# Performance work log

Measured on AMD Instinct MI355X. Metric: run time of the kernel, lower is better.

The kernel has to match this reference:

```python
import jax, jax.numpy as jnp
import numpy as np

S, B, D = 2048, 1, 4096
H, HKV, DH = 32, 8, 128
THETA = 10000.0


def _rope_tables(seq_len, dim, theta):
    inv_freq = 1.0 / (theta ** (jnp.arange(0, dim, 2, dtype=jnp.float32) / dim))
    freqs = jnp.arange(seq_len, dtype=jnp.float32)[:, None] * inv_freq[None, :]  # [S, DH/2]
    return jnp.cos(freqs), jnp.sin(freqs)


def _apply_rope(x, cos, sin):
    # x: [B, H, S, DH]; non-interleaved (flash_attn interleaved=False) rotation
    half = x.shape[-1] // 2
    x1, x2 = x[..., :half], x[..., half:]
    c = cos[None, None, :, :]
    s = sin[None, None, :, :]
    return jnp.concatenate([x1 * c - x2 * s, x2 * c + x1 * s], axis=-1)


def setup_inputs() -> dict:
    key = jax.random.key(0)
    k1, k2, k3 = jax.random.split(key, 3)
    hidden_states = jax.random.normal(k1, (S, B, D), dtype=jnp.float32)
    W_qkv = jax.random.normal(k2, (D, (H + 2 * HKV) * DH), dtype=jnp.float32) * 0.02
    W_o = jax.random.normal(k3, (H * DH, D), dtype=jnp.float32) * 0.02
    sequence_mask = jnp.ones((B, S), dtype=jnp.int32)
    return {"hidden_states": hidden_states, "sequence_mask": sequence_mask,
            "W_qkv": W_qkv, "W_o": W_o}


def reference(hidden_states, sequence_mask, W_qkv, W_o):
    s, b, _ = hidden_states.shape
    qkv = hidden_states @ W_qkv  # [S, B, (H+2*HKV)*DH]
    q, k, v = jnp.split(qkv, [H * DH, H * DH + HKV * DH], axis=-1)
    q = q.reshape(s, b, H, DH).transpose(1, 2, 0, 3)    # [B, H, S, DH]
    k = k.reshape(s, b, HKV, DH).transpose(1, 2, 0, 3)  # [B, HKV, S, DH]
    v = v.reshape(s, b, HKV, DH).transpose(1, 2, 0, 3)

    cos, sin = _rope_tables(s, DH, THETA)
    q = _apply_rope(q, cos, sin)
    k = _apply_rope(k, cos, sin)

    # GQA: repeat kv heads
    rep = H // HKV
    k = jnp.repeat(k, rep, axis=1)  # [B, H, S, DH]
    v = jnp.repeat(v, rep, axis=1)

    scale = 1.0 / jnp.sqrt(jnp.asarray(DH, dtype=q.dtype))
    scores = jnp.einsum('bhqd,bhkd->bhqk', q, k) * scale
    causal = jnp.tril(jnp.ones((s, s), dtype=bool))
    scores = jnp.where(causal[None, None, :, :], scores, jnp.finfo(scores.dtype).min)
    attn = jax.nn.softmax(scores, axis=-1)
    ctx = jnp.einsum('bhqk,bhkd->bhqd', attn, v)  # [B, H, S, DH]
    ctx = ctx.transpose(2, 0, 1, 3).reshape(s, b, H * DH)  # [S, B, H*DH]
    out = ctx @ W_o  # [S, B, D]
    return out
```

## Files before the change

kernel.cpp:

```cpp
#include <hip/hip_runtime.h>

typedef unsigned short u16;
typedef __bf16 bf16x8 __attribute__((ext_vector_type(8)));
typedef float f32x4 __attribute__((ext_vector_type(4)));
typedef u16 u16x4 __attribute__((ext_vector_type(4)));

constexpr int SEQ = 2048;
constexpr int NQKV = 6144;

__device__ __forceinline__ float bf2f(u16 x) {
    unsigned int u = ((unsigned int)x) << 16;
    return __builtin_bit_cast(float, u);
}
__device__ __forceinline__ u16 f2bf(float f) {
    unsigned int u = __builtin_bit_cast(unsigned int, f);
    u += 0x7FFF + ((u >> 16) & 1);
    return (u16)(u >> 16);
}

__device__ __forceinline__ void gload16(const void* g, void* l) {
    void* gg = const_cast<void*>(g);
    __builtin_amdgcn_global_load_lds(
        (__attribute__((address_space(1))) void*)gg,
        (__attribute__((address_space(3))) void*)l, 16, 0, 0);
}

__device__ __forceinline__ void gatebar(int G) {
    if (G == 8) asm volatile("s_waitcnt vmcnt(8)" ::: "memory");
    else if (G == 4) asm volatile("s_waitcnt vmcnt(4)" ::: "memory");
    else asm volatile("s_waitcnt vmcnt(0)" ::: "memory");
    __builtin_amdgcn_sched_barrier(0);
    __builtin_amdgcn_s_barrier();
    __builtin_amdgcn_sched_barrier(0);
}

__global__ void rope_table_k(float* __restrict__ tab) {
    int idx = blockIdx.x * 256 + threadIdx.x;
    if (idx >= SEQ * 64) return;
    int s = idx >> 6;
    int i = idx & 63;
    float invf = expf(-(float)i * (float)(1.0 / 64.0) * logf(10000.0f));
    float ang = (float)s * invf;
    float sv, cv;
    sincosf(ang, &sv, &cv);
    tab[idx * 2] = cv;
    tab[idx * 2 + 1] = sv;
}

__global__ __launch_bounds__(256) void cast_k(const float* __restrict__ src,
                                              u16* __restrict__ dst, int n4) {
    int i = blockIdx.x * 256 + threadIdx.x;
    if (i >= n4) return;
    f32x4 v = *(const f32x4*)&src[(size_t)i * 4];
    u16x4 o;
#pragma unroll
    for (int j = 0; j < 4; ++j) o[j] = f2bf(v[j]);
    *(u16x4*)&dst[(size_t)i * 4] = o;
}

__global__ __launch_bounds__(256) void transpose_cast_k(const float* __restrict__ src,
                                                        u16* __restrict__ dst, int R, int C) {
    __shared__ u16 tile[64][65];
    int t = threadIdx.x;
    int bx = blockIdx.x, by = blockIdx.y;
    int r0 = by * 64, c0 = bx * 64;
#pragma unroll
    for (int it = 0; it < 4; ++it) {
        int row = it * 16 + (t >> 4);
        int col = (t & 15) * 4;
        f32x4 v = *(const f32x4*)&src[(size_t)(r0 + row) * C + c0 + col];
        tile[row][col] = f2bf(v[0]); tile[row][col + 1] = f2bf(v[1]);
        tile[row][col + 2] = f2bf(v[2]); tile[row][col + 3] = f2bf(v[3]);
    }
    __syncthreads();
#pragma unroll
    for (int it = 0; it < 4; ++it) {
        int orow = it * 16 + (t >> 4);
        int ocol = (t & 15) * 4;
        u16x4 v;
        v[0] = tile[ocol][orow]; v[1] = tile[ocol + 1][orow];
        v[2] = tile[ocol + 2][orow]; v[3] = tile[ocol + 3][orow];
        *(u16x4*)&dst[(size_t)(c0 + orow) * R + r0 + ocol] = v;
    }
}

__global__ __launch_bounds__(256) void transpose_vt_k(const u16* __restrict__ QKV,
                                                      u16* __restrict__ VTg) {
    __shared__ u16 tile[64][65];
    int t = threadIdx.x;
    int s0 = blockIdx.x * 64;
    int hv = blockIdx.y >> 1;
    int d0 = (blockIdx.y & 1) * 64;
    const u16* src = QKV + (size_t)s0 * NQKV + 5120 + hv * 128 + d0;
#pragma unroll
    for (int it = 0; it < 4; ++it) {
        int row = it * 16 + (t >> 4);
        int col = (t & 15) * 4;
        u16x4 v = *(const u16x4*)&src[(size_t)row * NQKV + col];
        tile[row][col] = v[0]; tile[row][col + 1] = v[1];
        tile[row][col + 2] = v[2]; tile[row][col + 3] = v[3];
    }
    __syncthreads();
    u16* dst = VTg + (size_t)hv * 128 * SEQ + (size_t)d0 * SEQ + s0;
#pragma unroll
    for (int it = 0; it < 4; ++it) {
        int orow = it * 16 + (t >> 4);
        int ocol = (t & 15) * 4;
        u16x4 v;
        v[0] = tile[ocol][orow]; v[1] = tile[ocol + 1][orow];
        v[2] = tile[ocol + 2][orow]; v[3] = tile[ocol + 3][orow];
        *(u16x4*)&dst[(size_t)orow * SEQ + ocol] = v;
    }
}

__global__ __launch_bounds__(512, 2) void gemm1_big_k(const u16* __restrict__ A,
                                                      const u16* __restrict__ BT,
                                                      u16* __restrict__ C) {
    constexpr int K = 4096, N = 6144;
    constexpr int SBUF = 57344;
    __shared__ alignas(16) char lds[2 * SBUF];

    int t = threadIdx.x;
    int lane = t & 63, w = t >> 6;
    int wr = w >> 2, wc = w & 3;
    int l15 = lane & 15, l4 = lane >> 4;

    int wg = blockIdx.x;
    int xcd = wg & 7, j = wg >> 3;
    int bm = ((xcd >> 2) << 2) + (j >> 3);
    int bn = ((xcd & 3) << 3) + (j & 7);

    const u16* Ab = A + (size_t)bm * 256 * K;
    const u16* Bb = BT + (size_t)bn * 192 * K;

    const u16* ga[4]; int da[4];
#pragma unroll
    for (int i = 0; i < 4; ++i) {
        int c = t + i * 512;
        int row = c >> 3;
        int ch = (c & 7) ^ (row & 7);
        ga[i] = Ab + (size_t)row * K + ch * 8;
        da[i] = c * 16;
    }
    const u16* gb[3]; int db[3];
#pragma unroll
    for (int i = 0; i < 3; ++i) {
        int c = t + i * 512;
        int row = c >> 3;
        int ch = (c & 7) ^ (row & 7);
        gb[i] = Bb + (size_t)row * K + ch * 8;
        db[i] = 32768 + c * 16;
    }

    auto stage = [&](int kt) {
        char* L = lds + (kt & 1) * SBUF;
        int ko = kt * 64;
#pragma unroll
        for (int i = 0; i < 4; ++i) gload16(ga[i] + ko, L + da[i]);
#pragma unroll
        for (int i = 0; i < 3; ++i) gload16(gb[i] + ko, L + db[i]);
    };

    f32x4 acc[8][3];
#pragma unroll
    for (int i = 0; i < 8; ++i)
#pragma unroll
        for (int j2 = 0; j2 < 3; ++j2) acc[i][j2] = f32x4{0.f, 0.f, 0.f, 0.f};

    int arow[8];
#pragma unroll
    for (int fm = 0; fm < 8; ++fm) arow[fm] = wr * 128 + fm * 16 + l15;
    int brow[3];
#pragma unroll
    for (int fn = 0; fn < 3; ++fn) brow[fn] = wc * 48 + fn * 16 + l15;

    stage(0);
    gatebar(0);

    for (int kt = 0; kt < 64; ++kt) {
        const u16* L = (const u16*)(lds + (kt & 1) * SBUF);
        if (kt + 1 < 64) stage(kt + 1);
        bf16x8 bf[3][2];
#pragma unroll
        for (int fn = 0; fn < 3; ++fn)
#pragma unroll
            for (int kk = 0; kk < 2; ++kk) {
                int ch = (kk * 4 + l4) ^ (brow[fn] & 7);
                bf[fn][kk] = *(const bf16x8*)&L[16384 + brow[fn] * 64 + ch * 8];
            }
#pragma unroll
        for (int p = 0; p < 4; ++p) {
            bf16x8 af[2][2];
#pragma unroll
            for (int f2 = 0; f2 < 2; ++f2)
#pragma unroll
                for (int kk = 0; kk < 2; ++kk) {
                    int r = arow[p * 2 + f2];
                    int ch = (kk * 4 + l4) ^ (r & 7);
                    af[f2][kk] = *(const bf16x8*)&L[r * 64 + ch * 8];
                }
            __builtin_amdgcn_s_setprio(1);
#pragma unroll
            for (int f2 = 0; f2 < 2; ++f2)
#pragma unroll
                for (int kk = 0; kk < 2; ++kk)
#pragma unroll
                    for (int fn = 0; fn < 3; ++fn)
                        acc[p * 2 + f2][fn] = __builtin_amdgcn_mfma_f32_16x16x32_bf16(
                            af[f2][kk], bf[fn][kk], acc[p * 2 + f2][fn], 0, 0, 0);
            __builtin_amdgcn_s_setprio(0);
        }
        gatebar(0);
    }

#pragma unroll
    for (int fm = 0; fm < 8; ++fm)
#pragma unroll
        for (int fn = 0; fn < 3; ++fn)
#pragma unroll
            for (int i = 0; i < 4; ++i) {
                int row = bm * 256 + wr * 128 + fm * 16 + l4 * 4 + i;
                int col = bn * 192 + wc * 48 + fn * 16 + l15;
                C[(size_t)row * N + col] = f2bf(acc[fm][fn][i]);
            }
}

__global__ __launch_bounds__(512, 2) void gemm2_big_k(const u16* __restrict__ A,
                                                      const u16* __restrict__ BT,
                                                      float* __restrict__ C) {
    constexpr int K = 4096, N = 4096;
    constexpr int SBUF = 49152;
    __shared__ alignas(16) char lds[2 * SBUF];

    int t = threadIdx.x;
    int lane = t & 63, w = t >> 6;
    int wr = w >> 2, wc = w & 3;
    int l15 = lane & 15, l4 = lane >> 4;

    int wg = blockIdx.x;
    int xcd = wg & 7, j = wg >> 3;
    int bm = ((xcd >> 2) << 2) + (j >> 3);
    int bn = ((xcd & 3) << 3) + (j & 7);

    const u16* Ab = A + (size_t)bm * 256 * K;
    const u16* Bb = BT + (size_t)bn * 128 * K;

    const u16* ga[4]; int da[4];
#pragma unroll
    for (int i = 0; i < 4; ++i) {
        int c = t + i * 512;
        int row = c >> 3;
        int ch = (c & 7) ^ (row & 7);
        ga[i] = Ab + (size_t)row * K + ch * 8;
        da[i] = c * 16;
    }
    const u16* gb[2]; int db[2];
#pragma unroll
    for (int i = 0; i < 2; ++i) {
        int c = t + i * 512;
        int row = c >> 3;
        int ch = (c & 7) ^ (row & 7);
        gb[i] = Bb + (size_t)row * K + ch * 8;
        db[i] = 32768 + c * 16;
    }

    auto stage = [&](int kt) {
        char* L = lds + (kt & 1) * SBUF;
        int ko = kt * 64;
#pragma unroll
        for (int i = 0; i < 4; ++i) gload16(ga[i] + ko, L + da[i]);
#pragma unroll
        for (int i = 0; i < 2; ++i) gload16(gb[i] + ko, L + db[i]);
    };

    f32x4 acc[8][2];
#pragma unroll
    for (int i = 0; i < 8; ++i)
#pragma unroll
        for (int j2 = 0; j2 < 2; ++j2) acc[i][j2] = f32x4{0.f, 0.f, 0.f, 0.f};

    int arow[8];
#pragma unroll
    for (int fm = 0; fm < 8; ++fm) arow[fm] = wr * 128 + fm * 16 + l15;
    int brow[2];
#pragma unroll
    for (int fn = 0; fn < 2; ++fn) brow[fn] = wc * 32 + fn * 16 + l15;

    stage(0);
    gatebar(0);

    for (int kt = 0; kt < 64; ++kt) {
        const u16* L = (const u16*)(lds + (kt & 1) * SBUF);
        if (kt + 1 < 64) stage(kt + 1);
        bf16x8 bf[2][2];
#pragma unroll
        for (int fn = 0; fn < 2; ++fn)
#pragma unroll
            for (int kk = 0; kk < 2; ++kk) {
                int ch = (kk * 4 + l4) ^ (brow[fn] & 7);
                bf[fn][kk] = *(const bf16x8*)&L[16384 + brow[fn] * 64 + ch * 8];
            }
#pragma unroll
        for (int p = 0; p < 4; ++p) {
            bf16x8 af[2][2];
#pragma unroll
            for (int f2 = 0; f2 < 2; ++f2)
#pragma unroll
                for (int kk = 0; kk < 2; ++kk) {
                    int r = arow[p * 2 + f2];
                    int ch = (kk * 4 + l4) ^ (r & 7);
                    af[f2][kk] = *(const bf16x8*)&L[r * 64 + ch * 8];
                }
            __builtin_amdgcn_s_setprio(1);
#pragma unroll
            for (int f2 = 0; f2 < 2; ++f2)
#pragma unroll
                for (int kk = 0; kk < 2; ++kk)
#pragma unroll
                    for (int fn = 0; fn < 2; ++fn)
                        acc[p * 2 + f2][fn] = __builtin_amdgcn_mfma_f32_16x16x32_bf16(
                            af[f2][kk], bf[fn][kk], acc[p * 2 + f2][fn], 0, 0, 0);
            __builtin_amdgcn_s_setprio(0);
        }
        gatebar(0);
    }

#pragma unroll
    for (int fm = 0; fm < 8; ++fm)
#pragma unroll
        for (int fn = 0; fn < 2; ++fn)
#pragma unroll
            for (int i = 0; i < 4; ++i) {
                int row = bm * 256 + wr * 128 + fm * 16 + l4 * 4 + i;
                int col = bn * 128 + wc * 32 + fn * 16 + l15;
                C[(size_t)row * N + col] = acc[fm][fn][i];
            }
}

__global__ __launch_bounds__(256) void repack_rope_k(const u16* __restrict__ QKV,
                                                     const float* __restrict__ tab,
                                                     u16* __restrict__ Qo, u16* __restrict__ Ko) {
    int idx = blockIdx.x * 256 + threadIdx.x;
    int i4 = (idx & 15) * 4;
    int su = idx >> 4;
    int u = su % 40;
    int s = su / 40;
    const float* tp = tab + (s * 64 + i4) * 2;
    f32x4 t0 = *(const f32x4*)tp;
    f32x4 t1 = *(const f32x4*)(tp + 4);
    float cv[4] = {t0[0], t0[2], t1[0], t1[2]};
    float sv[4] = {t0[1], t0[3], t1[1], t1[3]};
    const u16* base;
    u16* ob;
    if (u < 32) {
        base = QKV + (size_t)s * NQKV + u * 128;
        ob = Qo + ((size_t)u * SEQ + s) * 128;
    } else {
        base = QKV + (size_t)s * NQKV + 4096 + (u - 32) * 128;
        ob = Ko + ((size_t)(u - 32) * SEQ + s) * 128;
    }
    u16x4 x1 = *(const u16x4*)(base + i4);
    u16x4 x2 = *(const u16x4*)(base + 64 + i4);
    u16x4 o1, o2;
#pragma unroll
    for (int j = 0; j < 4; ++j) {
        float a = bf2f(x1[j]), b = bf2f(x2[j]);
        o1[j] = f2bf(a * cv[j] - b * sv[j]);
        o2[j] = f2bf(b * cv[j] + a * sv[j]);
    }
    *(u16x4*)(ob + i4) = o1;
    *(u16x4*)(ob + 64 + i4) = o2;
}

__global__ __launch_bounds__(512) void attn_k(const u16* __restrict__ Qg,
                                              const u16* __restrict__ Kg,
                                              const u16* __restrict__ VTg,
                                              u16* __restrict__ ctx) {
    constexpr float SCL2 = 0.08838834764831845f * 1.44269504088896340736f;
    constexpr float THR = 11.5f;
    __shared__ alignas(16) u16 Klds[2][128 * 128];
    __shared__ alignas(16) u16 VTl[2][128 * 128];
    __shared__ alignas(16) u16 Plds[8 * 16 * 72];

    int t = threadIdx.x;
    int lane = t & 63, w = t >> 6;
    int l15 = lane & 15, l4 = lane >> 4;
    int bx = blockIdx.x;
    int h = blockIdx.y, hkv = h >> 2;
    const u16* Kh = Kg + (size_t)hkv * SEQ * 128;
    const u16* Vh = VTg + (size_t)hkv * 128 * SEQ;
    u16* Pw = &Plds[w * 1152];

    int kr[4], kchs[4];
#pragma unroll
    for (int i2 = 0; i2 < 4; ++i2) {
        int c = t + i2 * 512;
        kr[i2] = c >> 4;
        kchs[i2] = (c & 15) ^ (kr[i2] & 7);
    }
    int vd[4], vchs[4];
#pragma unroll
    for (int i2 = 0; i2 < 4; ++i2) {
        int c = t + i2 * 512;
        vd[i2] = c >> 4;
        vchs[i2] = (c & 15) ^ (vd[i2] & 7);
    }

    int q0 = bx * 128;
    int ntA = bx + 1;

    bf16x8 qf[4];
    f32x4 o[8];
    float m_i[4], l_i[4];

    auto kvbase = [&](int tt) { return (tt < ntA ? tt : tt - ntA) << 7; };
    auto load_q = [&]() {
        const u16* Qh = Qg + ((size_t)h * SEQ + q0 + w * 16 + l15) * 128;
#pragma unroll
        for (int ks = 0; ks < 4; ++ks) qf[ks] = *(const bf16x8*)(Qh + ks * 32 + l4 * 8);
    };
    auto reset_acc = [&]() {
#pragma unroll
        for (int nf = 0; nf < 8; ++nf) o[nf] = f32x4{0.f, 0.f, 0.f, 0.f};
#pragma unroll
        for (int i = 0; i < 4; ++i) { m_i[i] = -3.0e38f; l_i[i] = 0.f; }
    };
    auto write_ctx = [&]() {
        float inv[4];
#pragma unroll
        for (int i = 0; i < 4; ++i) {
            float rs = l_i[i];
            rs += __shfl_xor(rs, 1);
            rs += __shfl_xor(rs, 2);
            rs += __shfl_xor(rs, 4);
            rs += __shfl_xor(rs, 8);
            inv[i] = 1.0f / rs;
        }
#pragma unroll
        for (int nf = 0; nf < 8; ++nf)
#pragma unroll
            for (int i = 0; i < 4; ++i) {
                int qrow = q0 + w * 16 + l4 * 4 + i;
                ctx[(size_t)qrow * 4096 + h * 128 + nf * 16 + l15] = f2bf(o[nf][i] * inv[i]);
            }
    };
    auto stage = [&](int tt) {
        int kv0 = kvbase(tt);
        const u16* Kt = Kh + (size_t)kv0 * 128;
        char* kb = (char*)Klds[tt & 1];
        char* vb = (char*)VTl[tt & 1];
#pragma unroll
        for (int i2 = 0; i2 < 4; ++i2)
            gload16(Kt + kr[i2] * 128 + kchs[i2] * 8, kb + (size_t)(t + i2 * 512) * 16);
#pragma unroll
        for (int i2 = 0; i2 < 4; ++i2)
            gload16(Vh + (size_t)vd[i2] * SEQ + kv0 + vchs[i2] * 8,
                    vb + (size_t)(t + i2 * 512) * 16);
    };

    load_q();
    reset_acc();
    stage(0);

    for (int tt = 0; tt < 17; ++tt) {
        __builtin_amdgcn_s_barrier();
        __builtin_amdgcn_sched_barrier(0);
        bool nxt = (tt + 1 < 17);
        if (nxt) stage(tt + 1);
        gatebar(nxt ? 8 : 0);
        if (tt == ntA) {
            write_ctx();
            q0 = (15 - bx) * 128;
            load_q();
            reset_acc();
        }

        int b = tt & 1;
        int kv0 = kvbase(tt);
        const u16* KL = Klds[b];
        const u16* VL = VTl[b];

        f32x4 sa[8];
#pragma unroll
        for (int cg = 0; cg < 8; ++cg) {
            sa[cg] = f32x4{0.f, 0.f, 0.f, 0.f};
            int row = cg * 16 + l15;
#pragma unroll
            for (int ks = 0; ks < 4; ++ks) {
                int chs = (ks * 4 + l4) ^ (row & 7);
                bf16x8 kf = *(const bf16x8*)&KL[row * 128 + chs * 8];
                sa[cg] = __builtin_amdgcn_mfma_f32_16x16x32_bf16(qf[ks], kf, sa[cg], 0, 0, 0);
            }
        }
#pragma unroll
        for (int cg = 0; cg < 8; ++cg)
#pragma unroll
            for (int i = 0; i < 4; ++i) sa[cg][i] *= SCL2;
        if (kv0 + 127 > q0 + w * 16) {
#pragma unroll
            for (int cg = 0; cg < 8; ++cg) {
                int col = kv0 + cg * 16 + l15;
#pragma unroll
                for (int i = 0; i < 4; ++i) {
                    int qrow = q0 + w * 16 + l4 * 4 + i;
                    if (col > qrow) sa[cg][i] = -3.0e38f;
                }
            }
        }
        float lmx[4];
#pragma unroll
        for (int i = 0; i < 4; ++i) {
            float a0 = fmaxf(fmaxf(sa[0][i], sa[1][i]), fmaxf(sa[2][i], sa[3][i]));
            float a1 = fmaxf(fmaxf(sa[4][i], sa[5][i]), fmaxf(sa[6][i], sa[7][i]));
            lmx[i] = fmaxf(a0, a1);
        }
        bool defer = __all((lmx[0] <= m_i[0] + THR) & (lmx[1] <= m_i[1] + THR) &
                           (lmx[2] <= m_i[2] + THR) & (lmx[3] <= m_i[3] + THR));
        if (!defer) {
            float corr[4];
#pragma unroll
            for (int i = 0; i < 4; ++i) {
                float m0 = lmx[i];
                m0 = fmaxf(m0, __shfl_xor(m0, 1));
                m0 = fmaxf(m0, __shfl_xor(m0, 2));
                m0 = fmaxf(m0, __shfl_xor(m0, 4));
                m0 = fmaxf(m0, __shfl_xor(m0, 8));
                float mnew = fmaxf(m_i[i], m0);
                corr[i] = __builtin_amdgcn_exp2f(m_i[i] - mnew);
                m_i[i] = mnew;
                l_i[i] *= corr[i];
            }
#pragma unroll
            for (int nf = 0; nf < 8; ++nf) {
                o[nf][0] *= corr[0]; o[nf][1] *= corr[1];
                o[nf][2] *= corr[2]; o[nf][3] *= corr[3];
            }
        }
#pragma unroll
        for (int hf = 0; hf < 2; ++hf) {
#pragma unroll
            for (int i = 0; i < 4; ++i) {
                int prow = l4 * 4 + i;
                int sw = (prow >> 1) & 3;
                float rs = 0.f;
#pragma unroll
                for (int cg = 0; cg < 4; ++cg) {
                    float p = __builtin_amdgcn_exp2f(sa[hf * 4 + cg][i] - m_i[i]);
                    rs += p;
                    int ch = cg * 2 + (l15 >> 3);
                    Pw[prow * 72 + ((ch ^ sw) << 3) + (l15 & 7)] = f2bf(p);
                }
                l_i[i] += rs;
            }
            asm volatile("s_waitcnt lgkmcnt(0)" ::: "memory");
            __builtin_amdgcn_sched_barrier(0);
#pragma unroll
            for (int kst = 0; kst < 2; ++kst) {
                int pchs = (kst * 4 + l4) ^ ((l15 >> 1) & 3);
                bf16x8 pf = *(const bf16x8*)&Pw[l15 * 72 + pchs * 8];
                int kst2 = hf * 2 + kst;
#pragma unroll
                for (int nf = 0; nf < 8; ++nf) {
                    int d = nf * 16 + l15;
                    int vch = (kst2 * 4 + l4) ^ (d & 7);
                    bf16x8 vf = *(const bf16x8*)&VL[d * 128 + vch * 8];
                    o[nf] = __builtin_amdgcn_mfma_f32_16x16x32_bf16(pf, vf, o[nf], 0, 0, 0);
                }
            }
        }
    }
    write_ctx();
}

extern "C" void kernel_launch(void* const* d_in, const int* in_sizes, int n_in,
                              void* d_out, int out_size, void* d_ws, size_t ws_size,
                              hipStream_t stream) {
    const float* hidden = (const float*)d_in[0];
    const float* Wqkv = (const float*)d_in[2];
    const float* Wo = (const float*)d_in[3];
    float* out = (float*)d_out;
    char* ws = (char*)d_ws;

    u16* WqkvT   = (u16*)(ws + 0);
    u16* Qb      = (u16*)(ws + 0);
    u16* Kb      = (u16*)(ws + 16777216);
    u16* VTg     = (u16*)(ws + 20971520);
    u16* WoT     = (u16*)(ws + 25165824);
    u16* QKV     = (u16*)(ws + 50331648);
    u16* ctx     = (u16*)(ws + 58720256);
    float* tab   = (float*)(ws + 75497472);
    u16* hiddenB = (u16*)(ws + 76546048);

    rope_table_k<<<512, 256, 0, stream>>>(tab);
    cast_k<<<8192, 256, 0, stream>>>(hidden, hiddenB, 2048 * 4096 / 4);
    transpose_cast_k<<<dim3(96, 64), 256, 0, stream>>>(Wqkv, WqkvT, 4096, 6144);
    gemm1_big_k<<<256, 512, 0, stream>>>(hiddenB, WqkvT, QKV);
    repack_rope_k<<<5120, 256, 0, stream>>>(QKV, tab, Qb, Kb);
    transpose_vt_k<<<dim3(32, 16), 256, 0, stream>>>(QKV, VTg);
    transpose_cast_k<<<dim3(64, 64), 256, 0, stream>>>(Wo, WoT, 4096, 4096);
    attn_k<<<dim3(8, 32), 512, 0, stream>>>(Qb, Kb, VTg, ctx);
    gemm2_big_k<<<256, 512, 0, stream>>>(ctx, WoT, out);
}
```

Measured before the change: 304.1 us.

## Fuse Q RoPE into attention load and reshape GEMM warp tiling

Q rotary embedding is now applied inside the attention kernel's Q load, read straight from the QKV buffer. The repack kernel therefore only handles K heads, which removes a write and re-read of a 16MB Q buffer. Separately, both GEMMs change their 8-warp layout from 2x4 to 4x2. Each warp now owns a squarer sub-tile, which changes the ratio of LDS fragment reads to MFMAs and raises per-warp accumulator register use. The workspace layout is reshuffled, and the rope table is now built after the first GEMM.

```diff
diff --git a/kernel.cpp b/kernel.cpp
--- a/kernel.cpp
+++ b/kernel.cpp
@@ -122,7 +122,7 @@
 
     int t = threadIdx.x;
     int lane = t & 63, w = t >> 6;
-    int wr = w >> 2, wc = w & 3;
+    int wr = w >> 1, wc = w & 1;
     int l15 = lane & 15, l4 = lane >> 4;
 
     int wg = blockIdx.x;
@@ -161,18 +161,18 @@
         for (int i = 0; i < 3; ++i) gload16(gb[i] + ko, L + db[i]);
     };
 
-    f32x4 acc[8][3];
-#pragma unroll
-    for (int i = 0; i < 8; ++i)
-#pragma unroll
-        for (int j2 = 0; j2 < 3; ++j2) acc[i][j2] = f32x4{0.f, 0.f, 0.f, 0.f};
-
-    int arow[8];
-#pragma unroll
-    for (int fm = 0; fm < 8; ++fm) arow[fm] = wr * 128 + fm * 16 + l15;
-    int brow[3];
-#pragma unroll
-    for (int fn = 0; fn < 3; ++fn) brow[fn] = wc * 48 + fn * 16 + l15;
+    f32x4 acc[4][6];
+#pragma unroll
+    for (int i = 0; i < 4; ++i)
+#pragma unroll
+        for (int j2 = 0; j2 < 6; ++j2) acc[i][j2] = f32x4{0.f, 0.f, 0.f, 0.f};
+
+    int arow[4];
+#pragma unroll
+    for (int fm = 0; fm < 4; ++fm) arow[fm] = wr * 64 + fm * 16 + l15;
+    int brow[6];
+#pragma unroll
+    for (int fn = 0; fn < 6; ++fn) brow[fn] = wc * 96 + fn * 16 + l15;
 
     stage(0);
     gatebar(0);
@@ -180,16 +180,16 @@
     for (int kt = 0; kt < 64; ++kt) {
         const u16* L = (const u16*)(lds + (kt & 1) * SBUF);
         if (kt + 1 < 64) stage(kt + 1);
-        bf16x8 bf[3][2];
-#pragma unroll
-        for (int fn = 0; fn < 3; ++fn)
+        bf16x8 bf[6][2];
+#pragma unroll
+        for (int fn = 0; fn < 6; ++fn)
 #pragma unroll
             for (int kk = 0; kk < 2; ++kk) {
                 int ch = (kk * 4 + l4) ^ (brow[fn] & 7);
                 bf[fn][kk] = *(const bf16x8*)&L[16384 + brow[fn] * 64 + ch * 8];
             }
 #pragma unroll
-        for (int p = 0; p < 4; ++p) {
+        for (int p = 0; p < 2; ++p) {
             bf16x8 af[2][2];
 #pragma unroll
             for (int f2 = 0; f2 < 2; ++f2)
@@ -205,7 +205,7 @@
 #pragma unroll
                 for (int kk = 0; kk < 2; ++kk)
 #pragma unroll
-                    for (int fn = 0; fn < 3; ++fn)
+                    for (int fn = 0; fn < 6; ++fn)
                         acc[p * 2 + f2][fn] = __builtin_amdgcn_mfma_f32_16x16x32_bf16(
                             af[f2][kk], bf[fn][kk], acc[p * 2 + f2][fn], 0, 0, 0);
             __builtin_amdgcn_s_setprio(0);
@@ -214,13 +214,13 @@
     }
 
 #pragma unroll
-    for (int fm = 0; fm < 8; ++fm)
-#pragma unroll
-        for (int fn = 0; fn < 3; ++fn)
+    for (int fm = 0; fm < 4; ++fm)
+#pragma unroll
+        for (int fn = 0; fn < 6; ++fn)
 #pragma unroll
             for (int i = 0; i < 4; ++i) {
-                int row = bm * 256 + wr * 128 + fm * 16 + l4 * 4 + i;
-                int col = bn * 192 + wc * 48 + fn * 16 + l15;
+                int row = bm * 256 + wr * 64 + fm * 16 + l4 * 4 + i;
+                int col = bn * 192 + wc * 96 + fn * 16 + l15;
                 C[(size_t)row * N + col] = f2bf(acc[fm][fn][i]);
             }
 }
@@ -234,7 +234,7 @@
 
     int t = threadIdx.x;
     int lane = t & 63, w = t >> 6;
-    int wr = w >> 2, wc = w & 3;
+    int wr = w >> 1, wc = w & 1;
     int l15 = lane & 15, l4 = lane >> 4;
 
     int wg = blockIdx.x;
@@ -273,18 +273,18 @@
         for (int i = 0; i < 2; ++i) gload16(gb[i] + ko, L + db[i]);
     };
 
-    f32x4 acc[8][2];
-#pragma unroll
-    for (int i = 0; i < 8; ++i)
-#pragma unroll
-        for (int j2 = 0; j2 < 2; ++j2) acc[i][j2] = f32x4{0.f, 0.f, 0.f, 0.f};
-
-    int arow[8];
-#pragma unroll
-    for (int fm = 0; fm < 8; ++fm) arow[fm] = wr * 128 + fm * 16 + l15;
-    int brow[2];
-#pragma unroll
-    for (int fn = 0; fn < 2; ++fn) brow[fn] = wc * 32 + fn * 16 + l15;
+    f32x4 acc[4][4];
+#pragma unroll
+    for (int i = 0; i < 4; ++i)
+#pragma unroll
+        for (int j2 = 0; j2 < 4; ++j2) acc[i][j2] = f32x4{0.f, 0.f, 0.f, 0.f};
+
+    int arow[4];
+#pragma unroll
+    for (int fm = 0; fm < 4; ++fm) arow[fm] = wr * 64 + fm * 16 + l15;
+    int brow[4];
+#pragma unroll
+    for (int fn = 0; fn < 4; ++fn) brow[fn] = wc * 64 + fn * 16 + l15;
 
     stage(0);
     gatebar(0);
@@ -292,16 +292,16 @@
     for (int kt = 0; kt < 64; ++kt) {
         const u16* L = (const u16*)(lds + (kt & 1) * SBUF);
         if (kt + 1 < 64) stage(kt + 1);
-        bf16x8 bf[2][2];
-#pragma unroll
-        for (int fn = 0; fn < 2; ++fn)
+        bf16x8 bf[4][2];
+#pragma unroll
+        for (int fn = 0; fn < 4; ++fn)
 #pragma unroll
             for (int kk = 0; kk < 2; ++kk) {
                 int ch = (kk * 4 + l4) ^ (brow[fn] & 7);
                 bf[fn][kk] = *(const bf16x8*)&L[16384 + brow[fn] * 64 + ch * 8];
             }
 #pragma unroll
-        for (int p = 0; p < 4; ++p) {
+        for (int p = 0; p < 2; ++p) {
             bf16x8 af[2][2];
 #pragma unroll
             for (int f2 = 0; f2 < 2; ++f2)
@@ -317,7 +317,7 @@
 #pragma unroll
                 for (int kk = 0; kk < 2; ++kk)
 #pragma unroll
-                    for (int fn = 0; fn < 2; ++fn)
+                    for (int fn = 0; fn < 4; ++fn)
                         acc[p * 2 + f2][fn] = __builtin_amdgcn_mfma_f32_16x16x32_bf16(
                             af[f2][kk], bf[fn][kk], acc[p * 2 + f2][fn], 0, 0, 0);
             __builtin_amdgcn_s_setprio(0);
@@ -326,39 +326,32 @@
     }
 
 #pragma unroll
-    for (int fm = 0; fm < 8; ++fm)
-#pragma unroll
-        for (int fn = 0; fn < 2; ++fn)
+    for (int fm = 0; fm < 4; ++fm)
+#pragma unroll
+        for (int fn = 0; fn < 4; ++fn)
 #pragma unroll
             for (int i = 0; i < 4; ++i) {
-                int row = bm * 256 + wr * 128 + fm * 16 + l4 * 4 + i;
-                int col = bn * 128 + wc * 32 + fn * 16 + l15;
+                int row = bm * 256 + wr * 64 + fm * 16 + l4 * 4 + i;
+                int col = bn * 128 + wc * 64 + fn * 16 + l15;
                 C[(size_t)row * N + col] = acc[fm][fn][i];
             }
 }
 
 __global__ __launch_bounds__(256) void repack_rope_k(const u16* __restrict__ QKV,
                                                      const float* __restrict__ tab,
-                                                     u16* __restrict__ Qo, u16* __restrict__ Ko) {
+                                                     u16* __restrict__ Ko) {
     int idx = blockIdx.x * 256 + threadIdx.x;
     int i4 = (idx & 15) * 4;
     int su = idx >> 4;
-    int u = su % 40;
-    int s = su / 40;
+    int u = su & 7;
+    int s = su >> 3;
     const float* tp = tab + (s * 64 + i4) * 2;
     f32x4 t0 = *(const f32x4*)tp;
     f32x4 t1 = *(const f32x4*)(tp + 4);
     float cv[4] = {t0[0], t0[2], t1[0], t1[2]};
     float sv[4] = {t0[1], t0[3], t1[1], t1[3]};
-    const u16* base;
-    u16* ob;
-    if (u < 32) {
-        base = QKV + (size_t)s * NQKV + u * 128;
-        ob = Qo + ((size_t)u * SEQ + s) * 128;
-    } else {
-        base = QKV + (size_t)s * NQKV + 4096 + (u - 32) * 128;
-        ob = Ko + ((size_t)(u - 32) * SEQ + s) * 128;
-    }
+    const u16* base = QKV + (size_t)s * NQKV + 4096 + u * 128;
+    u16* ob = Ko + ((size_t)u * SEQ + s) * 128;
     u16x4 x1 = *(const u16x4*)(base + i4);
     u16x4 x2 = *(const u16x4*)(base + 64 + i4);
     u16x4 o1, o2;
@@ -372,9 +365,10 @@
     *(u16x4*)(ob + 64 + i4) = o2;
 }
 
-__global__ __launch_bounds__(512) void attn_k(const u16* __restrict__ Qg,
+__global__ __launch_bounds__(512) void attn_k(const u16* __restrict__ QKVg,
                                               const u16* __restrict__ Kg,
                                               const u16* __restrict__ VTg,
+                                              const float* __restrict__ tab,
                                               u16* __restrict__ ctx) {
     constexpr float SCL2 = 0.08838834764831845f * 1.44269504088896340736f;
     constexpr float THR = 11.5f;
@@ -415,9 +409,40 @@
 
     auto kvbase = [&](int tt) { return (tt < ntA ? tt : tt - ntA) << 7; };
     auto load_q = [&]() {
-        const u16* Qh = Qg + ((size_t)h * SEQ + q0 + w * 16 + l15) * 128;
-#pragma unroll
-        for (int ks = 0; ks < 4; ++ks) qf[ks] = *(const bf16x8*)(Qh + ks * 32 + l4 * 8);
+        int s = q0 + w * 16 + l15;
+        const u16* Qh = QKVg + (size_t)s * NQKV + h * 128;
+        bf16x8 raw[4];
+#pragma unroll
+        for (int ks = 0; ks < 4; ++ks) raw[ks] = *(const bf16x8*)(Qh + ks * 32 + l4 * 8);
+        const float* tp0 = tab + ((size_t)s * 64 + l4 * 8) * 2;
+        const float* tp1 = tp0 + 64;
+        float c0[8], s0[8], c1[8], s1[8];
+#pragma unroll
+        for (int v4 = 0; v4 < 4; ++v4) {
+            f32x4 a = *(const f32x4*)(tp0 + v4 * 4);
+            c0[v4 * 2] = a[0]; s0[v4 * 2] = a[1];
+            c0[v4 * 2 + 1] = a[2]; s0[v4 * 2 + 1] = a[3];
+            f32x4 b2 = *(const f32x4*)(tp1 + v4 * 4);
+            c1[v4 * 2] = b2[0]; s1[v4 * 2] = b2[1];
+            c1[v4 * 2 + 1] = b2[2]; s1[v4 * 2 + 1] = b2[3];
+        }
+        const u16* r0 = (const u16*)&raw[0];
+        const u16* r1 = (const u16*)&raw[1];
+        const u16* r2 = (const u16*)&raw[2];
+        const u16* r3 = (const u16*)&raw[3];
+        u16* q0p = (u16*)&qf[0];
+        u16* q1p = (u16*)&qf[1];
+        u16* q2p = (u16*)&qf[2];
+        u16* q3p = (u16*)&qf[3];
+#pragma unroll
+        for (int j = 0; j < 8; ++j) {
+            float x0 = bf2f(r0[j]), x1 = bf2f(r1[j]);
+            float x2 = bf2f(r2[j]), x3 = bf2f(r3[j]);
+            q0p[j] = f2bf(x0 * c0[j] - x2 * s0[j]);
+            q2p[j] = f2bf(x2 * c0[j] + x0 * s0[j]);
+            q1p[j] = f2bf(x1 * c1[j] - x3 * s1[j]);
+            q3p[j] = f2bf(x3 * c1[j] + x1 * s1[j]);
+        }
     };
     auto reset_acc = [&]() {
 #pragma unroll
@@ -581,23 +606,22 @@
     float* out = (float*)d_out;
     char* ws = (char*)d_ws;
 
-    u16* WqkvT   = (u16*)(ws + 0);
-    u16* Qb      = (u16*)(ws + 0);
-    u16* Kb      = (u16*)(ws + 16777216);
-    u16* VTg     = (u16*)(ws + 20971520);
-    u16* WoT     = (u16*)(ws + 25165824);
-    u16* QKV     = (u16*)(ws + 50331648);
-    u16* ctx     = (u16*)(ws + 58720256);
-    float* tab   = (float*)(ws + 75497472);
-    u16* hiddenB = (u16*)(ws + 76546048);
-
-    rope_table_k<<<512, 256, 0, stream>>>(tab);
+    u16* QKV     = (u16*)(ws + 0);
+    u16* WqkvT   = (u16*)(ws + 25165824);
+    u16* Kb      = (u16*)(ws + 25165824);
+    u16* VTg     = (u16*)(ws + 29360128);
+    float* tab   = (float*)(ws + 33554432);
+    u16* WoT     = (u16*)(ws + 34603008);
+    u16* ctx     = (u16*)(ws + 68157440);
+    u16* hiddenB = (u16*)(ws + 75497472);
+
     cast_k<<<8192, 256, 0, stream>>>(hidden, hiddenB, 2048 * 4096 / 4);
     transpose_cast_k<<<dim3(96, 64), 256, 0, stream>>>(Wqkv, WqkvT, 4096, 6144);
     gemm1_big_k<<<256, 512, 0, stream>>>(hiddenB, WqkvT, QKV);
-    repack_rope_k<<<5120, 256, 0, stream>>>(QKV, tab, Qb, Kb);
+    rope_table_k<<<512, 256, 0, stream>>>(tab);
+    repack_rope_k<<<1024, 256, 0, stream>>>(QKV, tab, Kb);
     transpose_vt_k<<<dim3(32, 16), 256, 0, stream>>>(QKV, VTg);
     transpose_cast_k<<<dim3(64, 64), 256, 0, stream>>>(Wo, WoT, 4096, 4096);
-    attn_k<<<dim3(8, 32), 512, 0, stream>>>(Qb, Kb, VTg, ctx);
+    attn_k<<<dim3(8, 32), 512, 0, stream>>>(QKV, Kb, VTg, tab, ctx);
     gemm2_big_k<<<256, 512, 0, stream>>>(ctx, WoT, out);
 }
```

Measured after the change: 296.8 us. 2.4% less time.
